# Performance work log

Measured on AMD Instinct MI355X. Metric: run time of the kernel, lower is better.

The kernel has to match this reference:

```python
import jax, jax.numpy as jnp
import numpy as np

N_NODES = 100000
N_EDGES = 1600000
IN_CH, HID_CH, LAT = 32, 32, 16


def _gcn_layer(h, W, b, src, dst, norm):
    # PyG GCNConv: h' = scatter_add(norm * (h W)[src] -> dst) + b
    h = h @ W                                   # [N, out]
    msg = h[src] * norm[:, None]                # [E+N, out] gather
    out = jax.ops.segment_sum(msg, dst, num_segments=N_NODES)
    return out + b


def setup_inputs() -> dict:
    key = jax.random.key(0)
    ks = jax.random.split(key, 8)
    x = jax.random.normal(ks[0], (N_NODES, IN_CH), dtype=jnp.float32)
    edge_index = jax.random.randint(ks[1], (2, N_EDGES), 0, N_NODES, dtype=jnp.int32)
    def glorot(k, fan_in, fan_out):
        lim = np.sqrt(6.0 / (fan_in + fan_out)).astype(np.float32)
        return jax.random.uniform(k, (fan_in, fan_out), jnp.float32, -lim, lim)
    return {
        "x": x,
        "edge_index": edge_index,
        "W1": glorot(ks[2], IN_CH, HID_CH),
        "b1": jnp.zeros((HID_CH,), jnp.float32),
        "Wmu": glorot(ks[3], HID_CH, LAT),
        "bmu": jnp.zeros((LAT,), jnp.float32),
        "Wlv": glorot(ks[4], HID_CH, LAT),
        "blv": jnp.zeros((LAT,), jnp.float32),
    }


def reference(x, edge_index, W1, b1, Wmu, bmu, Wlv, blv):
    # Add self-loops (GCNConv default add_self_loops=True)
    loops = jnp.arange(N_NODES, dtype=edge_index.dtype)
    src = jnp.concatenate([edge_index[0], loops])
    dst = jnp.concatenate([edge_index[1], loops])
    # Symmetric normalization: deg over destinations, norm = d^-1/2[src] * d^-1/2[dst]
    deg = jax.ops.segment_sum(jnp.ones_like(dst, dtype=x.dtype), dst,
                              num_segments=N_NODES)
    dinv = jnp.where(deg > 0, jax.lax.rsqrt(deg), 0.0)
    norm = dinv[src] * dinv[dst]                # [E+N]

    h = jax.nn.relu(_gcn_layer(x, W1, b1, src, dst, norm))
    mu = _gcn_layer(h, Wmu, bmu, src, dst, norm)
    logvar = _gcn_layer(h, Wlv, blv, src, dst, norm)
    return (mu, logvar)
```

## Files before the change

kernel.cpp:

```cpp
#include <hip/hip_runtime.h>
#include <hip/hip_fp16.h>

#define N_NODES 100000
#define N_EDGES 1600000
#define NCB 98
#define CAPC 17500
#define P1_CHUNK 2048
#define P1_BLOCKS 782
#define BK 64
#define NBF 1563
#define CAPF 1408
#define P2_SPLIT 16

__global__ __launch_bounds__(1024) void k_binit(int* __restrict__ cursor1,
                                                int* __restrict__ cursor2) {
    int i = blockIdx.x * 1024 + threadIdx.x;
    if (i < NCB) cursor1[i] = i * CAPC;
    if (i < NBF) cursor2[i] = i * CAPF;
}

__global__ __launch_bounds__(256) void k_part1(const int* __restrict__ src,
                                               const int* __restrict__ dst,
                                               int* __restrict__ cursor1,
                                               unsigned* __restrict__ packed1) {
    __shared__ int bh[NCB];
    __shared__ int base[NCB];
    int t = threadIdx.x;
    if (t < NCB) bh[t] = 0;
    __syncthreads();
    int e0 = blockIdx.x * P1_CHUNK;
    int e1 = e0 + P1_CHUNK; if (e1 > N_EDGES) e1 = N_EDGES;
    for (int e = e0 + t; e < e1; e += 256)
        atomicAdd(&bh[((unsigned)dst[e]) >> 10], 1);
    __syncthreads();
    if (t < NCB) {
        int c = bh[t];
        base[t] = (c > 0) ? atomicAdd(&cursor1[t], c) : 0;
        bh[t] = 0;
    }
    __syncthreads();
    for (int e = e0 + t; e < e1; e += 256) {
        unsigned d = (unsigned)dst[e];
        int b = d >> 10;
        int r = atomicAdd(&bh[b], 1);
        int pos = base[b] + r;
        if (pos < (b + 1) * CAPC)
            packed1[pos] = ((d & 1023u) << 17) | (unsigned)src[e];
    }
}

__global__ __launch_bounds__(256) void k_part2(const unsigned* __restrict__ packed1,
                                               const int* __restrict__ cursor1,
                                               int* __restrict__ cursor2,
                                               unsigned* __restrict__ packed2) {
    __shared__ int bh[16];
    __shared__ int base[16];
    int t = threadIdx.x;
    int c = blockIdx.x / P2_SPLIT;
    int k = blockIdx.x % P2_SPLIT;
    int cc = cursor1[c] - c * CAPC; if (cc > CAPC) cc = CAPC;
    int s0 = c * CAPC + (k * cc) / P2_SPLIT;
    int s1 = c * CAPC + ((k + 1) * cc) / P2_SPLIT;
    if (t < 16) bh[t] = 0;
    __syncthreads();
    for (int i = s0 + t; i < s1; i += 256)
        atomicAdd(&bh[(packed1[i] >> 17) >> 6], 1);
    __syncthreads();
    if (t < 16) {
        int cnt = bh[t];
        int fb = c * 16 + t;
        base[t] = (cnt > 0) ? atomicAdd(&cursor2[fb], cnt) : 0;
        bh[t] = 0;
    }
    __syncthreads();
    for (int i = s0 + t; i < s1; i += 256) {
        unsigned pk = packed1[i];
        unsigned dl = pk >> 17;
        int f = dl >> 6;
        int r = atomicAdd(&bh[f], 1);
        int pos = base[f] + r;
        int fb = c * 16 + f;
        if (pos < (fb + 1) * CAPF)
            packed2[pos] = ((dl & 63u) << 17) | (pk & 0x1FFFFu);
    }
}

__global__ __launch_bounds__(256) void k_csrx(const unsigned* __restrict__ packed2,
                                              const int* __restrict__ cursor2,
                                              const float* __restrict__ x,
                                              const float* __restrict__ W1,
                                              int* __restrict__ rowBeg,
                                              int* __restrict__ rowEnd,
                                              float* __restrict__ dinv,
                                              int* __restrict__ srcSorted,
                                              __half* __restrict__ p1) {
    __shared__ int cnt[BK];
    __shared__ int s[BK];
    __shared__ int cur[BK];
    __shared__ float sW[32 * 32];
    int t = threadIdx.x;
    int b = blockIdx.x;
    int seg0 = b * CAPF;
    int cc = cursor2[b] - seg0; if (cc > CAPF) cc = CAPF;
    int segEnd = seg0 + cc;
    if (t < BK) cnt[t] = 0;
    for (int i = t; i < 1024; i += 256) sW[i] = W1[i];
    __syncthreads();
    for (int i = seg0 + t; i < segEnd; i += 256)
        atomicAdd(&cnt[packed2[i] >> 17], 1);
    __syncthreads();
    int v = (t < BK) ? cnt[t] : 0;
    if (t < BK) s[t] = v;
    __syncthreads();
    for (int off = 1; off < BK; off <<= 1) {
        int u = (t < BK && t >= off) ? s[t - off] : 0;
        __syncthreads();
        if (t < BK) s[t] += u;
        __syncthreads();
    }
    int node = b * BK + t;
    if (t < BK) {
        int start = seg0 + s[t] - v;
        if (node < N_NODES) {
            rowBeg[node] = start;
            rowEnd[node] = start + v;
            dinv[node] = rsqrtf((float)(v + 1));
        }
        cur[t] = start;
    }
    __syncthreads();
    for (int i = seg0 + t; i < segEnd; i += 256) {
        unsigned pk = packed2[i];
        int pos = atomicAdd(&cur[pk >> 17], 1);
        srcSorted[pos] = (int)(pk & 0x1FFFFu);
    }
    int lane = t & 31;
    for (int r = (t >> 5); r < BK; r += 8) {
        int nd = b * BK + r;
        if (nd > N_NODES) break;
        if (nd == N_NODES) {
            p1[nd * 32 + lane] = __float2half(0.f);
            continue;
        }
        float xv = x[nd * 32 + lane];
        float a = 0.f;
#pragma unroll
        for (int k = 0; k < 32; ++k) {
            float xk = __shfl(xv, k, 32);
            a += xk * sW[k * 32 + lane];
        }
        float di = rsqrtf((float)(cnt[r] + 1));
        p1[nd * 32 + lane] = __float2half(di * a);
    }
}

__device__ __forceinline__ __half2 h2of(const float4& v, int c) {
    return reinterpret_cast<const __half2*>(&v)[c];
}

__device__ __forceinline__ void gatherRow4(const int* __restrict__ srcSorted,
                                           const float4* __restrict__ P,
                                           int beg, int end, int l,
                                           float* __restrict__ acc ) {
    for (int base = beg; base < end; base += 8) {
        int i0 = base + l, i1 = base + 4 + l;
        int sA = (i0 < end) ? srcSorted[i0] : N_NODES;
        int sB = (i1 < end) ? srcSorted[i1] : N_NODES;
        float4 v0 = P[__shfl(sA, 0, 4) * 4 + l];
        float4 v1 = P[__shfl(sA, 1, 4) * 4 + l];
        float4 v2 = P[__shfl(sA, 2, 4) * 4 + l];
        float4 v3 = P[__shfl(sA, 3, 4) * 4 + l];
        float4 v4 = P[__shfl(sB, 0, 4) * 4 + l];
        float4 v5 = P[__shfl(sB, 1, 4) * 4 + l];
        float4 v6 = P[__shfl(sB, 2, 4) * 4 + l];
        float4 v7 = P[__shfl(sB, 3, 4) * 4 + l];
#pragma unroll
        for (int c = 0; c < 4; ++c) {
            __half2 s01 = __hadd2(h2of(v0, c), h2of(v1, c));
            __half2 s23 = __hadd2(h2of(v2, c), h2of(v3, c));
            __half2 s45 = __hadd2(h2of(v4, c), h2of(v5, c));
            __half2 s67 = __hadd2(h2of(v6, c), h2of(v7, c));
            __half2 sum = __hadd2(__hadd2(s01, s23), __hadd2(s45, s67));
            float2 f = __half22float2(sum);
            acc[2 * c]     += f.x;
            acc[2 * c + 1] += f.y;
        }
    }
}

__global__ __launch_bounds__(256) void k_gx2(const int* __restrict__ rowBeg,
                                             const int* __restrict__ rowEnd,
                                             const int* __restrict__ srcSorted,
                                             const __half* __restrict__ p1,
                                             const float* __restrict__ dinv,
                                             const float* __restrict__ b1,
                                             const float* __restrict__ Wmu,
                                             const float* __restrict__ Wlv,
                                             __half* __restrict__ p2) {
    __shared__ float sW[32 * 32];
    __shared__ float sB[32];
    int t = threadIdx.x;
    for (int i = t; i < 1024; i += 256) {
        int k = i >> 5, oc = i & 31;
        sW[i] = (oc < 16) ? Wmu[k * 16 + oc] : Wlv[k * 16 + (oc - 16)];
    }
    if (t < 32) sB[t] = b1[t];
    __syncthreads();
    int l = t & 3;
    int node = blockIdx.x * 64 + (t >> 2);
    if (node > N_NODES) return;
    const float4* P = (const float4*)p1;
    if (node == N_NODES) {
        ((float4*)p2)[node * 4 + l] = make_float4(0.f, 0.f, 0.f, 0.f);
        return;
    }
    float acc[8] = {0.f, 0.f, 0.f, 0.f, 0.f, 0.f, 0.f, 0.f};
    gatherRow4(srcSorted, P, rowBeg[node], rowEnd[node], l, acc);
    float di = dinv[node];
    float4 ps = P[node * 4 + l];
    float h[8];
#pragma unroll
    for (int c = 0; c < 4; ++c) {
        float2 f = __half22float2(h2of(ps, c));
        h[2 * c]     = fmaxf(di * (acc[2 * c]     + f.x) + sB[8 * l + 2 * c],     0.f);
        h[2 * c + 1] = fmaxf(di * (acc[2 * c + 1] + f.y) + sB[8 * l + 2 * c + 1], 0.f);
    }
    float o[8] = {0.f, 0.f, 0.f, 0.f, 0.f, 0.f, 0.f, 0.f};
    const float4* W4 = (const float4*)sW;
#pragma unroll
    for (int m = 0; m < 4; ++m) {
#pragma unroll
        for (int j = 0; j < 8; ++j) {
            float hk = __shfl(h[j], m, 4);
            int k = 8 * m + j;
            float4 wa = W4[k * 8 + 2 * l];
            float4 wb = W4[k * 8 + 2 * l + 1];
            o[0] += hk * wa.x; o[1] += hk * wa.y; o[2] += hk * wa.z; o[3] += hk * wa.w;
            o[4] += hk * wb.x; o[5] += hk * wb.y; o[6] += hk * wb.z; o[7] += hk * wb.w;
        }
    }
    __half2 r0 = __floats2half2_rn(di * o[0], di * o[1]);
    __half2 r1 = __floats2half2_rn(di * o[2], di * o[3]);
    __half2 r2 = __floats2half2_rn(di * o[4], di * o[5]);
    __half2 r3 = __floats2half2_rn(di * o[6], di * o[7]);
    float4 st;
    st.x = *reinterpret_cast<float*>(&r0);
    st.y = *reinterpret_cast<float*>(&r1);
    st.z = *reinterpret_cast<float*>(&r2);
    st.w = *reinterpret_cast<float*>(&r3);
    ((float4*)p2)[node * 4 + l] = st;
}

__global__ __launch_bounds__(256) void k_gfin(const int* __restrict__ rowBeg,
                                              const int* __restrict__ rowEnd,
                                              const int* __restrict__ srcSorted,
                                              const __half* __restrict__ p2,
                                              const float* __restrict__ dinv,
                                              const float* __restrict__ bmu,
                                              const float* __restrict__ blv,
                                              float* __restrict__ out) {
    __shared__ float sB[32];
    int t = threadIdx.x;
    if (t < 32) sB[t] = (t < 16) ? bmu[t] : blv[t - 16];
    __syncthreads();
    int l = t & 3;
    int node = blockIdx.x * 64 + (t >> 2);
    if (node >= N_NODES) return;
    const float4* P = (const float4*)p2;
    float acc[8] = {0.f, 0.f, 0.f, 0.f, 0.f, 0.f, 0.f, 0.f};
    gatherRow4(srcSorted, P, rowBeg[node], rowEnd[node], l, acc);
    float di = dinv[node];
    float4 ps = P[node * 4 + l];
    float v[8];
#pragma unroll
    for (int c = 0; c < 4; ++c) {
        float2 f = __half22float2(h2of(ps, c));
        v[2 * c]     = di * (acc[2 * c]     + f.x) + sB[8 * l + 2 * c];
        v[2 * c + 1] = di * (acc[2 * c + 1] + f.y) + sB[8 * l + 2 * c + 1];
    }
    float4 o0 = make_float4(v[0], v[1], v[2], v[3]);
    float4 o1 = make_float4(v[4], v[5], v[6], v[7]);
    float4* dst = (l < 2) ? (float4*)out
                          : (float4*)(out + (size_t)N_NODES * 16);
    int base = node * 4 + (l & 1) * 2;
    dst[base]     = o0;
    dst[base + 1] = o1;
}

extern "C" void kernel_launch(void* const* d_in, const int* in_sizes, int n_in,
                              void* d_out, int out_size, void* d_ws, size_t ws_size,
                              hipStream_t stream) {
    const float* x   = (const float*)d_in[0];
    const int*   ei  = (const int*)d_in[1];
    const float* W1  = (const float*)d_in[2];
    const float* b1  = (const float*)d_in[3];
    const float* Wmu = (const float*)d_in[4];
    const float* bmu = (const float*)d_in[5];
    const float* Wlv = (const float*)d_in[6];
    const float* blv = (const float*)d_in[7];
    float* out = (float*)d_out;

    const int* src = ei;
    const int* dst = ei + N_EDGES;

    size_t off = 0;
    int* cursor1 = (int*)d_ws;                          off += NCB;
    int* cursor2 = (int*)d_ws + off;                    off += NBF;
    int* rowBeg  = (int*)d_ws + off;                    off += N_NODES;
    int* rowEnd  = (int*)d_ws + off;                    off += N_NODES;
    float* dinv  = (float*)((int*)d_ws + off);          off += N_NODES;
    off = (off + 63) & ~(size_t)63;
    unsigned* packed1 = (unsigned*)((int*)d_ws + off);  off += (size_t)NCB * CAPC;
    off = (off + 63) & ~(size_t)63;
    unsigned* packed2 = (unsigned*)((int*)d_ws + off);  off += (size_t)NBF * CAPF;
    off = (off + 63) & ~(size_t)63;
    int* srcSorted    = (int*)d_ws + off;
    __half* p1h       = (__half*)packed1;
    __half* p2h       = (__half*)packed2;

    const int gBlocks = 1563;

    k_binit<<<2, 1024, 0, stream>>>(cursor1, cursor2);
    k_part1<<<P1_BLOCKS, 256, 0, stream>>>(src, dst, cursor1, packed1);
    k_part2<<<NCB * P2_SPLIT, 256, 0, stream>>>(packed1, cursor1, cursor2, packed2);
    k_csrx <<<NBF, 256, 0, stream>>>(packed2, cursor2, x, W1,
                                     rowBeg, rowEnd, dinv, srcSorted, p1h);
    k_gx2  <<<gBlocks, 256, 0, stream>>>(rowBeg, rowEnd, srcSorted, p1h, dinv,
                                         b1, Wmu, Wlv, p2h);
    k_gfin <<<gBlocks, 256, 0, stream>>>(rowBeg, rowEnd, srcSorted, p2h, dinv,
                                         bmu, blv, out);
}
```

Baseline: 195.4 us.

## Fuse all stages into one cooperative persistent kernel with grid syncs

Combines cursor init, two partition passes, CSR build with the first linear transform, and both GCN gather layers into a single cooperatively launched kernel separated by grid-wide barriers. The grid is sized from the occupancy query and the CU count, and blocks loop over the former per-launch work items. This aims to remove inter-kernel launch gaps and tail effects. In exchange it adds grid.sync overhead, host-side occupancy queries each call, and possibly lower occupancy from the larger merged kernel. The old multi-kernel path is kept as a fallback if the cooperative launch fails.

After: 618.5 us. 3.16x slower.

```diff
diff --git a/kernel.cpp b/kernel.cpp
--- a/kernel.cpp
+++ b/kernel.cpp
@@ -1,158 +1,18 @@
 #include <hip/hip_runtime.h>
 #include <hip/hip_fp16.h>
+#include <hip/hip_cooperative_groups.h>
+
+namespace cg = cooperative_groups;
 
 #define N_NODES 100000
 #define N_EDGES 1600000
 #define NCB 98
 #define CAPC 17500
-#define P1_CHUNK 2048
-#define P1_BLOCKS 782
 #define BK 64
 #define NBF 1563
 #define CAPF 1408
-#define P2_SPLIT 16
-
-__global__ __launch_bounds__(1024) void k_binit(int* __restrict__ cursor1,
-                                                int* __restrict__ cursor2) {
-    int i = blockIdx.x * 1024 + threadIdx.x;
-    if (i < NCB) cursor1[i] = i * CAPC;
-    if (i < NBF) cursor2[i] = i * CAPF;
-}
-
-__global__ __launch_bounds__(256) void k_part1(const int* __restrict__ src,
-                                               const int* __restrict__ dst,
-                                               int* __restrict__ cursor1,
-                                               unsigned* __restrict__ packed1) {
-    __shared__ int bh[NCB];
-    __shared__ int base[NCB];
-    int t = threadIdx.x;
-    if (t < NCB) bh[t] = 0;
-    __syncthreads();
-    int e0 = blockIdx.x * P1_CHUNK;
-    int e1 = e0 + P1_CHUNK; if (e1 > N_EDGES) e1 = N_EDGES;
-    for (int e = e0 + t; e < e1; e += 256)
-        atomicAdd(&bh[((unsigned)dst[e]) >> 10], 1);
-    __syncthreads();
-    if (t < NCB) {
-        int c = bh[t];
-        base[t] = (c > 0) ? atomicAdd(&cursor1[t], c) : 0;
-        bh[t] = 0;
-    }
-    __syncthreads();
-    for (int e = e0 + t; e < e1; e += 256) {
-        unsigned d = (unsigned)dst[e];
-        int b = d >> 10;
-        int r = atomicAdd(&bh[b], 1);
-        int pos = base[b] + r;
-        if (pos < (b + 1) * CAPC)
-            packed1[pos] = ((d & 1023u) << 17) | (unsigned)src[e];
-    }
-}
-
-__global__ __launch_bounds__(256) void k_part2(const unsigned* __restrict__ packed1,
-                                               const int* __restrict__ cursor1,
-                                               int* __restrict__ cursor2,
-                                               unsigned* __restrict__ packed2) {
-    __shared__ int bh[16];
-    __shared__ int base[16];
-    int t = threadIdx.x;
-    int c = blockIdx.x / P2_SPLIT;
-    int k = blockIdx.x % P2_SPLIT;
-    int cc = cursor1[c] - c * CAPC; if (cc > CAPC) cc = CAPC;
-    int s0 = c * CAPC + (k * cc) / P2_SPLIT;
-    int s1 = c * CAPC + ((k + 1) * cc) / P2_SPLIT;
-    if (t < 16) bh[t] = 0;
-    __syncthreads();
-    for (int i = s0 + t; i < s1; i += 256)
-        atomicAdd(&bh[(packed1[i] >> 17) >> 6], 1);
-    __syncthreads();
-    if (t < 16) {
-        int cnt = bh[t];
-        int fb = c * 16 + t;
-        base[t] = (cnt > 0) ? atomicAdd(&cursor2[fb], cnt) : 0;
-        bh[t] = 0;
-    }
-    __syncthreads();
-    for (int i = s0 + t; i < s1; i += 256) {
-        unsigned pk = packed1[i];
-        unsigned dl = pk >> 17;
-        int f = dl >> 6;
-        int r = atomicAdd(&bh[f], 1);
-        int pos = base[f] + r;
-        int fb = c * 16 + f;
-        if (pos < (fb + 1) * CAPF)
-            packed2[pos] = ((dl & 63u) << 17) | (pk & 0x1FFFFu);
-    }
-}
-
-__global__ __launch_bounds__(256) void k_csrx(const unsigned* __restrict__ packed2,
-                                              const int* __restrict__ cursor2,
-                                              const float* __restrict__ x,
-                                              const float* __restrict__ W1,
-                                              int* __restrict__ rowBeg,
-                                              int* __restrict__ rowEnd,
-                                              float* __restrict__ dinv,
-                                              int* __restrict__ srcSorted,
-                                              __half* __restrict__ p1) {
-    __shared__ int cnt[BK];
-    __shared__ int s[BK];
-    __shared__ int cur[BK];
-    __shared__ float sW[32 * 32];
-    int t = threadIdx.x;
-    int b = blockIdx.x;
-    int seg0 = b * CAPF;
-    int cc = cursor2[b] - seg0; if (cc > CAPF) cc = CAPF;
-    int segEnd = seg0 + cc;
-    if (t < BK) cnt[t] = 0;
-    for (int i = t; i < 1024; i += 256) sW[i] = W1[i];
-    __syncthreads();
-    for (int i = seg0 + t; i < segEnd; i += 256)
-        atomicAdd(&cnt[packed2[i] >> 17], 1);
-    __syncthreads();
-    int v = (t < BK) ? cnt[t] : 0;
-    if (t < BK) s[t] = v;
-    __syncthreads();
-    for (int off = 1; off < BK; off <<= 1) {
-        int u = (t < BK && t >= off) ? s[t - off] : 0;
-        __syncthreads();
-        if (t < BK) s[t] += u;
-        __syncthreads();
-    }
-    int node = b * BK + t;
-    if (t < BK) {
-        int start = seg0 + s[t] - v;
-        if (node < N_NODES) {
-            rowBeg[node] = start;
-            rowEnd[node] = start + v;
-            dinv[node] = rsqrtf((float)(v + 1));
-        }
-        cur[t] = start;
-    }
-    __syncthreads();
-    for (int i = seg0 + t; i < segEnd; i += 256) {
-        unsigned pk = packed2[i];
-        int pos = atomicAdd(&cur[pk >> 17], 1);
-        srcSorted[pos] = (int)(pk & 0x1FFFFu);
-    }
-    int lane = t & 31;
-    for (int r = (t >> 5); r < BK; r += 8) {
-        int nd = b * BK + r;
-        if (nd > N_NODES) break;
-        if (nd == N_NODES) {
-            p1[nd * 32 + lane] = __float2half(0.f);
-            continue;
-        }
-        float xv = x[nd * 32 + lane];
-        float a = 0.f;
-#pragma unroll
-        for (int k = 0; k < 32; ++k) {
-            float xk = __shfl(xv, k, 32);
-            a += xk * sW[k * 32 + lane];
-        }
-        float di = rsqrtf((float)(cnt[r] + 1));
-        p1[nd * 32 + lane] = __float2half(di * a);
-    }
-}
+#define P1_CHUNK 2048
+#define NCH 782
 
 __device__ __forceinline__ __half2 h2of(const float4& v, int c) {
     return reinterpret_cast<const __half2*>(&v)[c];
@@ -188,6 +48,388 @@
     }
 }
 
+__global__ __launch_bounds__(256) void k_all(
+    const float* __restrict__ x,
+    const int* __restrict__ srcE,
+    const int* __restrict__ dstE,
+    const float* __restrict__ W1,
+    const float* __restrict__ b1,
+    const float* __restrict__ Wmu,
+    const float* __restrict__ bmu,
+    const float* __restrict__ Wlv,
+    const float* __restrict__ blv,
+    int* __restrict__ cursor1,
+    int* __restrict__ cursor2,
+    int* __restrict__ rowBeg,
+    int* __restrict__ rowEnd,
+    float* __restrict__ dinv,
+    unsigned* __restrict__ packed1,
+    unsigned* __restrict__ packed2,
+    int* __restrict__ srcSorted,
+    __half* __restrict__ p1,
+    __half* __restrict__ p2,
+    float* __restrict__ out)
+{
+    cg::grid_group grid = cg::this_grid();
+    __shared__ int bh[NCB];
+    __shared__ int base[NCB];
+    __shared__ int cnt[BK];
+    __shared__ int scn[BK];
+    __shared__ int cur[BK];
+    __shared__ float sW[1024];
+    __shared__ float sB[32];
+    int t = threadIdx.x;
+    int blk = blockIdx.x;
+    int G = gridDim.x;
+
+    for (int i = blk * 256 + t; i < NBF; i += G * 256) {
+        cursor2[i] = i * CAPF;
+        if (i < NCB) cursor1[i] = i * CAPC;
+    }
+    grid.sync();
+
+    for (int u = blk; u < NCH; u += G) {
+        __syncthreads();
+        if (t < NCB) bh[t] = 0;
+        __syncthreads();
+        int e0 = u * P1_CHUNK;
+        int e1 = e0 + P1_CHUNK; if (e1 > N_EDGES) e1 = N_EDGES;
+        for (int e = e0 + t; e < e1; e += 256)
+            atomicAdd(&bh[((unsigned)dstE[e]) >> 10], 1);
+        __syncthreads();
+        if (t < NCB) {
+            int c = bh[t];
+            base[t] = (c > 0) ? atomicAdd(&cursor1[t], c) : 0;
+            bh[t] = 0;
+        }
+        __syncthreads();
+        for (int e = e0 + t; e < e1; e += 256) {
+            unsigned d = (unsigned)dstE[e];
+            int b = d >> 10;
+            int r = atomicAdd(&bh[b], 1);
+            int pos = base[b] + r;
+            if (pos < (b + 1) * CAPC)
+                packed1[pos] = ((d & 1023u) << 17) | (unsigned)srcE[e];
+        }
+    }
+    grid.sync();
+
+    for (int u = blk; u < NCB * 16; u += G) {
+        __syncthreads();
+        int c = u >> 4;
+        int k = u & 15;
+        int cc = cursor1[c] - c * CAPC; if (cc > CAPC) cc = CAPC;
+        int s0 = c * CAPC + (k * cc) / 16;
+        int s1 = c * CAPC + ((k + 1) * cc) / 16;
+        if (t < 16) bh[t] = 0;
+        __syncthreads();
+        for (int i = s0 + t; i < s1; i += 256)
+            atomicAdd(&bh[(packed1[i] >> 17) >> 6], 1);
+        __syncthreads();
+        if (t < 16) {
+            int c2 = bh[t];
+            int fb = c * 16 + t;
+            base[t] = (c2 > 0) ? atomicAdd(&cursor2[fb], c2) : 0;
+            bh[t] = 0;
+        }
+        __syncthreads();
+        for (int i = s0 + t; i < s1; i += 256) {
+            unsigned pk = packed1[i];
+            unsigned dl = pk >> 17;
+            int f = dl >> 6;
+            int r = atomicAdd(&bh[f], 1);
+            int pos = base[f] + r;
+            int fb = c * 16 + f;
+            if (pos < (fb + 1) * CAPF)
+                packed2[pos] = ((dl & 63u) << 17) | (pk & 0x1FFFFu);
+        }
+    }
+    grid.sync();
+
+    for (int i = t; i < 1024; i += 256) sW[i] = W1[i];
+    for (int u = blk; u < NBF; u += G) {
+        __syncthreads();
+        if (t < BK) cnt[t] = 0;
+        __syncthreads();
+        int seg0 = u * CAPF;
+        int cc = cursor2[u] - seg0; if (cc > CAPF) cc = CAPF;
+        int segEnd = seg0 + cc;
+        for (int i = seg0 + t; i < segEnd; i += 256)
+            atomicAdd(&cnt[packed2[i] >> 17], 1);
+        __syncthreads();
+        int v = (t < BK) ? cnt[t] : 0;
+        if (t < BK) scn[t] = v;
+        __syncthreads();
+        for (int off = 1; off < BK; off <<= 1) {
+            int uu = (t < BK && t >= off) ? scn[t - off] : 0;
+            __syncthreads();
+            if (t < BK) scn[t] += uu;
+            __syncthreads();
+        }
+        int node = u * BK + t;
+        if (t < BK) {
+            int start = seg0 + scn[t] - v;
+            if (node < N_NODES) {
+                rowBeg[node] = start;
+                rowEnd[node] = start + v;
+                dinv[node] = rsqrtf((float)(v + 1));
+            }
+            cur[t] = start;
+        }
+        __syncthreads();
+        for (int i = seg0 + t; i < segEnd; i += 256) {
+            unsigned pk = packed2[i];
+            int pos = atomicAdd(&cur[pk >> 17], 1);
+            srcSorted[pos] = (int)(pk & 0x1FFFFu);
+        }
+        int lane = t & 31;
+        for (int r = (t >> 5); r < BK; r += 8) {
+            int nd = u * BK + r;
+            if (nd > N_NODES) break;
+            if (nd == N_NODES) {
+                p1[nd * 32 + lane] = __float2half(0.f);
+                continue;
+            }
+            float xv = x[nd * 32 + lane];
+            float a = 0.f;
+#pragma unroll
+            for (int k = 0; k < 32; ++k) {
+                float xk = __shfl(xv, k, 32);
+                a += xk * sW[k * 32 + lane];
+            }
+            float di = rsqrtf((float)(cnt[r] + 1));
+            p1[nd * 32 + lane] = __float2half(di * a);
+        }
+    }
+    grid.sync();
+
+    for (int i = t; i < 1024; i += 256) {
+        int k = i >> 5, oc = i & 31;
+        sW[i] = (oc < 16) ? Wmu[k * 16 + oc] : Wlv[k * 16 + (oc - 16)];
+    }
+    if (t < 32) sB[t] = b1[t];
+    __syncthreads();
+    {
+        int l = t & 3;
+        const float4* P = (const float4*)p1;
+        const float4* W4 = (const float4*)sW;
+        for (int u = blk; u < NBF; u += G) {
+            int node = u * 64 + (t >> 2);
+            if (node > N_NODES) continue;
+            if (node == N_NODES) {
+                ((float4*)p2)[node * 4 + l] = make_float4(0.f, 0.f, 0.f, 0.f);
+                continue;
+            }
+            float acc[8] = {0.f, 0.f, 0.f, 0.f, 0.f, 0.f, 0.f, 0.f};
+            gatherRow4(srcSorted, P, rowBeg[node], rowEnd[node], l, acc);
+            float di = dinv[node];
+            float4 ps = P[node * 4 + l];
+            float h[8];
+#pragma unroll
+            for (int c = 0; c < 4; ++c) {
+                float2 f = __half22float2(h2of(ps, c));
+                h[2 * c]     = fmaxf(di * (acc[2 * c]     + f.x) + sB[8 * l + 2 * c],     0.f);
+                h[2 * c + 1] = fmaxf(di * (acc[2 * c + 1] + f.y) + sB[8 * l + 2 * c + 1], 0.f);
+            }
+            float o[8] = {0.f, 0.f, 0.f, 0.f, 0.f, 0.f, 0.f, 0.f};
+#pragma unroll
+            for (int m = 0; m < 4; ++m) {
+#pragma unroll
+                for (int j = 0; j < 8; ++j) {
+                    float hk = __shfl(h[j], m, 4);
+                    int k = 8 * m + j;
+                    float4 wa = W4[k * 8 + 2 * l];
+                    float4 wb = W4[k * 8 + 2 * l + 1];
+                    o[0] += hk * wa.x; o[1] += hk * wa.y; o[2] += hk * wa.z; o[3] += hk * wa.w;
+                    o[4] += hk * wb.x; o[5] += hk * wb.y; o[6] += hk * wb.z; o[7] += hk * wb.w;
+                }
+            }
+            __half2 r0 = __floats2half2_rn(di * o[0], di * o[1]);
+            __half2 r1 = __floats2half2_rn(di * o[2], di * o[3]);
+            __half2 r2 = __floats2half2_rn(di * o[4], di * o[5]);
+            __half2 r3 = __floats2half2_rn(di * o[6], di * o[7]);
+            float4 st;
+            st.x = *reinterpret_cast<float*>(&r0);
+            st.y = *reinterpret_cast<float*>(&r1);
+            st.z = *reinterpret_cast<float*>(&r2);
+            st.w = *reinterpret_cast<float*>(&r3);
+            ((float4*)p2)[node * 4 + l] = st;
+        }
+    }
+    grid.sync();
+
+    if (t < 32) sB[t] = (t < 16) ? bmu[t] : blv[t - 16];
+    __syncthreads();
+    {
+        int l = t & 3;
+        const float4* P = (const float4*)p2;
+        for (int u = blk; u < NBF; u += G) {
+            int node = u * 64 + (t >> 2);
+            if (node >= N_NODES) continue;
+            float acc[8] = {0.f, 0.f, 0.f, 0.f, 0.f, 0.f, 0.f, 0.f};
+            gatherRow4(srcSorted, P, rowBeg[node], rowEnd[node], l, acc);
+            float di = dinv[node];
+            float4 ps = P[node * 4 + l];
+            float v[8];
+#pragma unroll
+            for (int c = 0; c < 4; ++c) {
+                float2 f = __half22float2(h2of(ps, c));
+                v[2 * c]     = di * (acc[2 * c]     + f.x) + sB[8 * l + 2 * c];
+                v[2 * c + 1] = di * (acc[2 * c + 1] + f.y) + sB[8 * l + 2 * c + 1];
+            }
+            float4 o0 = make_float4(v[0], v[1], v[2], v[3]);
+            float4 o1 = make_float4(v[4], v[5], v[6], v[7]);
+            float4* dst4 = (l < 2) ? (float4*)out
+                                   : (float4*)(out + (size_t)N_NODES * 16);
+            int b4 = node * 4 + (l & 1) * 2;
+            dst4[b4]     = o0;
+            dst4[b4 + 1] = o1;
+        }
+    }
+}
+
+__global__ __launch_bounds__(1024) void k_binit(int* __restrict__ cursor1,
+                                                int* __restrict__ cursor2) {
+    int i = blockIdx.x * 1024 + threadIdx.x;
+    if (i < NCB) cursor1[i] = i * CAPC;
+    if (i < NBF) cursor2[i] = i * CAPF;
+}
+
+__global__ __launch_bounds__(256) void k_part1(const int* __restrict__ src,
+                                               const int* __restrict__ dst,
+                                               int* __restrict__ cursor1,
+                                               unsigned* __restrict__ packed1) {
+    __shared__ int bh[NCB];
+    __shared__ int base[NCB];
+    int t = threadIdx.x;
+    if (t < NCB) bh[t] = 0;
+    __syncthreads();
+    int e0 = blockIdx.x * P1_CHUNK;
+    int e1 = e0 + P1_CHUNK; if (e1 > N_EDGES) e1 = N_EDGES;
+    for (int e = e0 + t; e < e1; e += 256)
+        atomicAdd(&bh[((unsigned)dst[e]) >> 10], 1);
+    __syncthreads();
+    if (t < NCB) {
+        int c = bh[t];
+        base[t] = (c > 0) ? atomicAdd(&cursor1[t], c) : 0;
+        bh[t] = 0;
+    }
+    __syncthreads();
+    for (int e = e0 + t; e < e1; e += 256) {
+        unsigned d = (unsigned)dst[e];
+        int b = d >> 10;
+        int r = atomicAdd(&bh[b], 1);
+        int pos = base[b] + r;
+        if (pos < (b + 1) * CAPC)
+            packed1[pos] = ((d & 1023u) << 17) | (unsigned)src[e];
+    }
+}
+
+__global__ __launch_bounds__(256) void k_part2(const unsigned* __restrict__ packed1,
+                                               const int* __restrict__ cursor1,
+                                               int* __restrict__ cursor2,
+                                               unsigned* __restrict__ packed2) {
+    __shared__ int bh[16];
+    __shared__ int base[16];
+    int t = threadIdx.x;
+    int c = blockIdx.x >> 4;
+    int k = blockIdx.x & 15;
+    int cc = cursor1[c] - c * CAPC; if (cc > CAPC) cc = CAPC;
+    int s0 = c * CAPC + (k * cc) / 16;
+    int s1 = c * CAPC + ((k + 1) * cc) / 16;
+    if (t < 16) bh[t] = 0;
+    __syncthreads();
+    for (int i = s0 + t; i < s1; i += 256)
+        atomicAdd(&bh[(packed1[i] >> 17) >> 6], 1);
+    __syncthreads();
+    if (t < 16) {
+        int cnt = bh[t];
+        int fb = c * 16 + t;
+        base[t] = (cnt > 0) ? atomicAdd(&cursor2[fb], cnt) : 0;
+        bh[t] = 0;
+    }
+    __syncthreads();
+    for (int i = s0 + t; i < s1; i += 256) {
+        unsigned pk = packed1[i];
+        unsigned dl = pk >> 17;
+        int f = dl >> 6;
+        int r = atomicAdd(&bh[f], 1);
+        int pos = base[f] + r;
+        int fb = c * 16 + f;
+        if (pos < (fb + 1) * CAPF)
+            packed2[pos] = ((dl & 63u) << 17) | (pk & 0x1FFFFu);
+    }
+}
+
+__global__ __launch_bounds__(256) void k_csrx(const unsigned* __restrict__ packed2,
+                                              const int* __restrict__ cursor2,
+                                              const float* __restrict__ x,
+                                              const float* __restrict__ W1,
+                                              int* __restrict__ rowBeg,
+                                              int* __restrict__ rowEnd,
+                                              float* __restrict__ dinv,
+                                              int* __restrict__ srcSorted,
+                                              __half* __restrict__ p1) {
+    __shared__ int cnt[BK];
+    __shared__ int scn[BK];
+    __shared__ int cur[BK];
+    __shared__ float sW[1024];
+    int t = threadIdx.x;
+    int b = blockIdx.x;
+    int seg0 = b * CAPF;
+    int cc = cursor2[b] - seg0; if (cc > CAPF) cc = CAPF;
+    int segEnd = seg0 + cc;
+    if (t < BK) cnt[t] = 0;
+    for (int i = t; i < 1024; i += 256) sW[i] = W1[i];
+    __syncthreads();
+    for (int i = seg0 + t; i < segEnd; i += 256)
+        atomicAdd(&cnt[packed2[i] >> 17], 1);
+    __syncthreads();
+    int v = (t < BK) ? cnt[t] : 0;
+    if (t < BK) scn[t] = v;
+    __syncthreads();
+    for (int off = 1; off < BK; off <<= 1) {
+        int u = (t < BK && t >= off) ? scn[t - off] : 0;
+        __syncthreads();
+        if (t < BK) scn[t] += u;
+        __syncthreads();
+    }
+    int node = b * BK + t;
+    if (t < BK) {
+        int start = seg0 + scn[t] - v;
+        if (node < N_NODES) {
+            rowBeg[node] = start;
+            rowEnd[node] = start + v;
+            dinv[node] = rsqrtf((float)(v + 1));
+        }
+        cur[t] = start;
+    }
+    __syncthreads();
+    for (int i = seg0 + t; i < segEnd; i += 256) {
+        unsigned pk = packed2[i];
+        int pos = atomicAdd(&cur[pk >> 17], 1);
+        srcSorted[pos] = (int)(pk & 0x1FFFFu);
+    }
+    int lane = t & 31;
+    for (int r = (t >> 5); r < BK; r += 8) {
+        int nd = b * BK + r;
+        if (nd > N_NODES) break;
+        if (nd == N_NODES) {
+            p1[nd * 32 + lane] = __float2half(0.f);
+            continue;
+        }
+        float xv = x[nd * 32 + lane];
+        float a = 0.f;
+#pragma unroll
+        for (int k = 0; k < 32; ++k) {
+            float xk = __shfl(xv, k, 32);
+            a += xk * sW[k * 32 + lane];
+        }
+        float di = rsqrtf((float)(cnt[r] + 1));
+        p1[nd * 32 + lane] = __float2half(di * a);
+    }
+}
+
 __global__ __launch_bounds__(256) void k_gx2(const int* __restrict__ rowBeg,
                                              const int* __restrict__ rowEnd,
                                              const int* __restrict__ srcSorted,
@@ -197,7 +439,7 @@
                                              const float* __restrict__ Wmu,
                                              const float* __restrict__ Wlv,
                                              __half* __restrict__ p2) {
-    __shared__ float sW[32 * 32];
+    __shared__ float sW[1024];
     __shared__ float sB[32];
     int t = threadIdx.x;
     for (int i = t; i < 1024; i += 256) {
@@ -280,11 +522,11 @@
     }
     float4 o0 = make_float4(v[0], v[1], v[2], v[3]);
     float4 o1 = make_float4(v[4], v[5], v[6], v[7]);
-    float4* dst = (l < 2) ? (float4*)out
-                          : (float4*)(out + (size_t)N_NODES * 16);
-    int base = node * 4 + (l & 1) * 2;
-    dst[base]     = o0;
-    dst[base + 1] = o1;
+    float4* dst4 = (l < 2) ? (float4*)out
+                           : (float4*)(out + (size_t)N_NODES * 16);
+    int b4 = node * 4 + (l & 1) * 2;
+    dst4[b4]     = o0;
+    dst4[b4 + 1] = o1;
 }
 
 extern "C" void kernel_launch(void* const* d_in, const int* in_sizes, int n_in,
@@ -318,15 +560,36 @@
     __half* p1h       = (__half*)packed1;
     __half* p2h       = (__half*)packed2;
 
-    const int gBlocks = 1563;
-
-    k_binit<<<2, 1024, 0, stream>>>(cursor1, cursor2);
-    k_part1<<<P1_BLOCKS, 256, 0, stream>>>(src, dst, cursor1, packed1);
-    k_part2<<<NCB * P2_SPLIT, 256, 0, stream>>>(packed1, cursor1, cursor2, packed2);
-    k_csrx <<<NBF, 256, 0, stream>>>(packed2, cursor2, x, W1,
-                                     rowBeg, rowEnd, dinv, srcSorted, p1h);
-    k_gx2  <<<gBlocks, 256, 0, stream>>>(rowBeg, rowEnd, srcSorted, p1h, dinv,
+    int dev = 0;
+    (void)hipGetDevice(&dev);
+    int numCU = 0;
+    (void)hipDeviceGetAttribute(&numCU, hipDeviceAttributeMultiprocessorCount, dev);
+    int occ = 0;
+    (void)hipOccupancyMaxActiveBlocksPerMultiprocessor(&occ, (const void*)k_all, 256, 0);
+    int grid = (numCU > 0 && occ > 0) ? numCU * occ : 0;
+    if (grid > 1568) grid = 1568;
+
+    hipError_t err = hipErrorUnknown;
+    if (grid > 0) {
+        void* kargs[] = {
+            (void*)&x, (void*)&src, (void*)&dst,
+            (void*)&W1, (void*)&b1, (void*)&Wmu, (void*)&bmu, (void*)&Wlv, (void*)&blv,
+            (void*)&cursor1, (void*)&cursor2, (void*)&rowBeg, (void*)&rowEnd, (void*)&dinv,
+            (void*)&packed1, (void*)&packed2, (void*)&srcSorted,
+            (void*)&p1h, (void*)&p2h, (void*)&out
+        };
+        err = hipLaunchCooperativeKernel((void*)k_all, dim3(grid), dim3(256),
+                                         kargs, 0, stream);
+    }
+    if (err != hipSuccess) {
+        k_binit<<<2, 1024, 0, stream>>>(cursor1, cursor2);
+        k_part1<<<NCH, 256, 0, stream>>>(src, dst, cursor1, packed1);
+        k_part2<<<NCB * 16, 256, 0, stream>>>(packed1, cursor1, cursor2, packed2);
+        k_csrx <<<NBF, 256, 0, stream>>>(packed2, cursor2, x, W1,
+                                         rowBeg, rowEnd, dinv, srcSorted, p1h);
+        k_gx2  <<<NBF, 256, 0, stream>>>(rowBeg, rowEnd, srcSorted, p1h, dinv,
                                          b1, Wmu, Wlv, p2h);
-    k_gfin <<<gBlocks, 256, 0, stream>>>(rowBeg, rowEnd, srcSorted, p2h, dinv,
+        k_gfin <<<NBF, 256, 0, stream>>>(rowBeg, rowEnd, srcSorted, p2h, dinv,
                                          bmu, blv, out);
-}
+    }
+}
```

## Drop second partition pass; CSR blocks filter their coarse bucket directly

Applied to the files above, without the earlier changes.

Removes the k_part2 kernel and the packed2 intermediate buffer. Each k_csrx block now scans the whole coarse bucket (about 16K entries) and keeps only the entries whose fine bucket matches its own, building the CSR directly from packed1. This saves one kernel launch plus a full write and read of the edge array. In exchange, each coarse bucket is read 16 times (twice per block), so global read traffic in the CSR kernel rises, though these reads likely hit L2.

Measured after the change: 226.6 us. +16.0%, slower.

```diff
diff --git a/kernel.cpp b/kernel.cpp
--- a/kernel.cpp
+++ b/kernel.cpp
@@ -6,153 +6,10 @@
 #define NCB 98
 #define CAPC 17500
 #define P1_CHUNK 2048
-#define P1_BLOCKS 782
+#define NCH 782
 #define BK 64
 #define NBF 1563
 #define CAPF 1408
-#define P2_SPLIT 16
-
-__global__ __launch_bounds__(1024) void k_binit(int* __restrict__ cursor1,
-                                                int* __restrict__ cursor2) {
-    int i = blockIdx.x * 1024 + threadIdx.x;
-    if (i < NCB) cursor1[i] = i * CAPC;
-    if (i < NBF) cursor2[i] = i * CAPF;
-}
-
-__global__ __launch_bounds__(256) void k_part1(const int* __restrict__ src,
-                                               const int* __restrict__ dst,
-                                               int* __restrict__ cursor1,
-                                               unsigned* __restrict__ packed1) {
-    __shared__ int bh[NCB];
-    __shared__ int base[NCB];
-    int t = threadIdx.x;
-    if (t < NCB) bh[t] = 0;
-    __syncthreads();
-    int e0 = blockIdx.x * P1_CHUNK;
-    int e1 = e0 + P1_CHUNK; if (e1 > N_EDGES) e1 = N_EDGES;
-    for (int e = e0 + t; e < e1; e += 256)
-        atomicAdd(&bh[((unsigned)dst[e]) >> 10], 1);
-    __syncthreads();
-    if (t < NCB) {
-        int c = bh[t];
-        base[t] = (c > 0) ? atomicAdd(&cursor1[t], c) : 0;
-        bh[t] = 0;
-    }
-    __syncthreads();
-    for (int e = e0 + t; e < e1; e += 256) {
-        unsigned d = (unsigned)dst[e];
-        int b = d >> 10;
-        int r = atomicAdd(&bh[b], 1);
-        int pos = base[b] + r;
-        if (pos < (b + 1) * CAPC)
-            packed1[pos] = ((d & 1023u) << 17) | (unsigned)src[e];
-    }
-}
-
-__global__ __launch_bounds__(256) void k_part2(const unsigned* __restrict__ packed1,
-                                               const int* __restrict__ cursor1,
-                                               int* __restrict__ cursor2,
-                                               unsigned* __restrict__ packed2) {
-    __shared__ int bh[16];
-    __shared__ int base[16];
-    int t = threadIdx.x;
-    int c = blockIdx.x / P2_SPLIT;
-    int k = blockIdx.x % P2_SPLIT;
-    int cc = cursor1[c] - c * CAPC; if (cc > CAPC) cc = CAPC;
-    int s0 = c * CAPC + (k * cc) / P2_SPLIT;
-    int s1 = c * CAPC + ((k + 1) * cc) / P2_SPLIT;
-    if (t < 16) bh[t] = 0;
-    __syncthreads();
-    for (int i = s0 + t; i < s1; i += 256)
-        atomicAdd(&bh[(packed1[i] >> 17) >> 6], 1);
-    __syncthreads();
-    if (t < 16) {
-        int cnt = bh[t];
-        int fb = c * 16 + t;
-        base[t] = (cnt > 0) ? atomicAdd(&cursor2[fb], cnt) : 0;
-        bh[t] = 0;
-    }
-    __syncthreads();
-    for (int i = s0 + t; i < s1; i += 256) {
-        unsigned pk = packed1[i];
-        unsigned dl = pk >> 17;
-        int f = dl >> 6;
-        int r = atomicAdd(&bh[f], 1);
-        int pos = base[f] + r;
-        int fb = c * 16 + f;
-        if (pos < (fb + 1) * CAPF)
-            packed2[pos] = ((dl & 63u) << 17) | (pk & 0x1FFFFu);
-    }
-}
-
-__global__ __launch_bounds__(256) void k_csrx(const unsigned* __restrict__ packed2,
-                                              const int* __restrict__ cursor2,
-                                              const float* __restrict__ x,
-                                              const float* __restrict__ W1,
-                                              int* __restrict__ rowBeg,
-                                              int* __restrict__ rowEnd,
-                                              float* __restrict__ dinv,
-                                              int* __restrict__ srcSorted,
-                                              __half* __restrict__ p1) {
-    __shared__ int cnt[BK];
-    __shared__ int s[BK];
-    __shared__ int cur[BK];
-    __shared__ float sW[32 * 32];
-    int t = threadIdx.x;
-    int b = blockIdx.x;
-    int seg0 = b * CAPF;
-    int cc = cursor2[b] - seg0; if (cc > CAPF) cc = CAPF;
-    int segEnd = seg0 + cc;
-    if (t < BK) cnt[t] = 0;
-    for (int i = t; i < 1024; i += 256) sW[i] = W1[i];
-    __syncthreads();
-    for (int i = seg0 + t; i < segEnd; i += 256)
-        atomicAdd(&cnt[packed2[i] >> 17], 1);
-    __syncthreads();
-    int v = (t < BK) ? cnt[t] : 0;
-    if (t < BK) s[t] = v;
-    __syncthreads();
-    for (int off = 1; off < BK; off <<= 1) {
-        int u = (t < BK && t >= off) ? s[t - off] : 0;
-        __syncthreads();
-        if (t < BK) s[t] += u;
-        __syncthreads();
-    }
-    int node = b * BK + t;
-    if (t < BK) {
-        int start = seg0 + s[t] - v;
-        if (node < N_NODES) {
-            rowBeg[node] = start;
-            rowEnd[node] = start + v;
-            dinv[node] = rsqrtf((float)(v + 1));
-        }
-        cur[t] = start;
-    }
-    __syncthreads();
-    for (int i = seg0 + t; i < segEnd; i += 256) {
-        unsigned pk = packed2[i];
-        int pos = atomicAdd(&cur[pk >> 17], 1);
-        srcSorted[pos] = (int)(pk & 0x1FFFFu);
-    }
-    int lane = t & 31;
-    for (int r = (t >> 5); r < BK; r += 8) {
-        int nd = b * BK + r;
-        if (nd > N_NODES) break;
-        if (nd == N_NODES) {
-            p1[nd * 32 + lane] = __float2half(0.f);
-            continue;
-        }
-        float xv = x[nd * 32 + lane];
-        float a = 0.f;
-#pragma unroll
-        for (int k = 0; k < 32; ++k) {
-            float xk = __shfl(xv, k, 32);
-            a += xk * sW[k * 32 + lane];
-        }
-        float di = rsqrtf((float)(cnt[r] + 1));
-        p1[nd * 32 + lane] = __float2half(di * a);
-    }
-}
 
 __device__ __forceinline__ __half2 h2of(const float4& v, int c) {
     return reinterpret_cast<const __half2*>(&v)[c];
@@ -188,6 +45,119 @@
     }
 }
 
+__global__ __launch_bounds__(128) void k_binit(int* __restrict__ cursor1) {
+    int t = threadIdx.x;
+    if (t < NCB) cursor1[t] = t * CAPC;
+}
+
+__global__ __launch_bounds__(256) void k_part1(const int* __restrict__ src,
+                                               const int* __restrict__ dst,
+                                               int* __restrict__ cursor1,
+                                               unsigned* __restrict__ packed1) {
+    __shared__ int bh[NCB];
+    __shared__ int base[NCB];
+    int t = threadIdx.x;
+    if (t < NCB) bh[t] = 0;
+    __syncthreads();
+    int e0 = blockIdx.x * P1_CHUNK;
+    int e1 = e0 + P1_CHUNK; if (e1 > N_EDGES) e1 = N_EDGES;
+    for (int e = e0 + t; e < e1; e += 256)
+        atomicAdd(&bh[((unsigned)dst[e]) >> 10], 1);
+    __syncthreads();
+    if (t < NCB) {
+        int c = bh[t];
+        base[t] = (c > 0) ? atomicAdd(&cursor1[t], c) : 0;
+        bh[t] = 0;
+    }
+    __syncthreads();
+    for (int e = e0 + t; e < e1; e += 256) {
+        unsigned d = (unsigned)dst[e];
+        int b = d >> 10;
+        int r = atomicAdd(&bh[b], 1);
+        int pos = base[b] + r;
+        if (pos < (b + 1) * CAPC)
+            packed1[pos] = ((d & 1023u) << 17) | (unsigned)src[e];
+    }
+}
+
+__global__ __launch_bounds__(256) void k_csrx(const unsigned* __restrict__ packed1,
+                                              const int* __restrict__ cursor1,
+                                              const float* __restrict__ x,
+                                              const float* __restrict__ W1,
+                                              int* __restrict__ rowBeg,
+                                              int* __restrict__ rowEnd,
+                                              float* __restrict__ dinv,
+                                              int* __restrict__ srcSorted,
+                                              __half* __restrict__ p1) {
+    __shared__ int cnt[BK];
+    __shared__ int scn[BK];
+    __shared__ int cur[BK];
+    __shared__ float sW[1024];
+    int t = threadIdx.x;
+    int b = blockIdx.x;
+    int c = b >> 4;
+    unsigned fl = (unsigned)(b & 15);
+    int seg0 = c * CAPC;
+    int cc = cursor1[c] - seg0; if (cc > CAPC) cc = CAPC;
+    int segEnd = seg0 + cc;
+    if (t < BK) cnt[t] = 0;
+    for (int i = t; i < 1024; i += 256) sW[i] = W1[i];
+    __syncthreads();
+    for (int i = seg0 + t; i < segEnd; i += 256) {
+        unsigned dl = packed1[i] >> 17;
+        if ((dl >> 6) == fl) atomicAdd(&cnt[dl & 63u], 1);
+    }
+    __syncthreads();
+    int v = (t < BK) ? cnt[t] : 0;
+    if (t < BK) scn[t] = v;
+    __syncthreads();
+    for (int off = 1; off < BK; off <<= 1) {
+        int u = (t < BK && t >= off) ? scn[t - off] : 0;
+        __syncthreads();
+        if (t < BK) scn[t] += u;
+        __syncthreads();
+    }
+    int fseg0 = b * CAPF;
+    int node = b * BK + t;
+    if (t < BK) {
+        int start = fseg0 + scn[t] - v;
+        if (node < N_NODES) {
+            rowBeg[node] = start;
+            rowEnd[node] = start + v;
+            dinv[node] = rsqrtf((float)(v + 1));
+        }
+        cur[t] = start;
+    }
+    __syncthreads();
+    for (int i = seg0 + t; i < segEnd; i += 256) {
+        unsigned pk = packed1[i];
+        unsigned dl = pk >> 17;
+        if ((dl >> 6) == fl) {
+            int pos = atomicAdd(&cur[dl & 63u], 1);
+            if (pos < (b + 1) * CAPF)
+                srcSorted[pos] = (int)(pk & 0x1FFFFu);
+        }
+    }
+    int lane = t & 31;
+    for (int r = (t >> 5); r < BK; r += 8) {
+        int nd = b * BK + r;
+        if (nd > N_NODES) break;
+        if (nd == N_NODES) {
+            p1[nd * 32 + lane] = __float2half(0.f);
+            continue;
+        }
+        float xv = x[nd * 32 + lane];
+        float a = 0.f;
+#pragma unroll
+        for (int k = 0; k < 32; ++k) {
+            float xk = __shfl(xv, k, 32);
+            a += xk * sW[k * 32 + lane];
+        }
+        float di = rsqrtf((float)(cnt[r] + 1));
+        p1[nd * 32 + lane] = __float2half(di * a);
+    }
+}
+
 __global__ __launch_bounds__(256) void k_gx2(const int* __restrict__ rowBeg,
                                              const int* __restrict__ rowEnd,
                                              const int* __restrict__ srcSorted,
@@ -197,7 +167,7 @@
                                              const float* __restrict__ Wmu,
                                              const float* __restrict__ Wlv,
                                              __half* __restrict__ p2) {
-    __shared__ float sW[32 * 32];
+    __shared__ float sW[1024];
     __shared__ float sB[32];
     int t = threadIdx.x;
     for (int i = t; i < 1024; i += 256) {
@@ -280,11 +250,11 @@
     }
     float4 o0 = make_float4(v[0], v[1], v[2], v[3]);
     float4 o1 = make_float4(v[4], v[5], v[6], v[7]);
-    float4* dst = (l < 2) ? (float4*)out
-                          : (float4*)(out + (size_t)N_NODES * 16);
-    int base = node * 4 + (l & 1) * 2;
-    dst[base]     = o0;
-    dst[base + 1] = o1;
+    float4* dst4 = (l < 2) ? (float4*)out
+                           : (float4*)(out + (size_t)N_NODES * 16);
+    int b4 = node * 4 + (l & 1) * 2;
+    dst4[b4]     = o0;
+    dst4[b4 + 1] = o1;
 }
 
 extern "C" void kernel_launch(void* const* d_in, const int* in_sizes, int n_in,
@@ -305,28 +275,23 @@
 
     size_t off = 0;
     int* cursor1 = (int*)d_ws;                          off += NCB;
-    int* cursor2 = (int*)d_ws + off;                    off += NBF;
     int* rowBeg  = (int*)d_ws + off;                    off += N_NODES;
     int* rowEnd  = (int*)d_ws + off;                    off += N_NODES;
     float* dinv  = (float*)((int*)d_ws + off);          off += N_NODES;
     off = (off + 63) & ~(size_t)63;
     unsigned* packed1 = (unsigned*)((int*)d_ws + off);  off += (size_t)NCB * CAPC;
     off = (off + 63) & ~(size_t)63;
-    unsigned* packed2 = (unsigned*)((int*)d_ws + off);  off += (size_t)NBF * CAPF;
+    int* srcSorted    = (int*)d_ws + off;               off += (size_t)NBF * CAPF;
     off = (off + 63) & ~(size_t)63;
-    int* srcSorted    = (int*)d_ws + off;
-    __half* p1h       = (__half*)packed1;
-    __half* p2h       = (__half*)packed2;
-
-    const int gBlocks = 1563;
-
-    k_binit<<<2, 1024, 0, stream>>>(cursor1, cursor2);
-    k_part1<<<P1_BLOCKS, 256, 0, stream>>>(src, dst, cursor1, packed1);
-    k_part2<<<NCB * P2_SPLIT, 256, 0, stream>>>(packed1, cursor1, cursor2, packed2);
-    k_csrx <<<NBF, 256, 0, stream>>>(packed2, cursor2, x, W1,
+    __half* p1h       = (__half*)((int*)d_ws + off);
+    __half* p2h       = (__half*)packed1;
+
+    k_binit<<<1, 128, 0, stream>>>(cursor1);
+    k_part1<<<NCH, 256, 0, stream>>>(src, dst, cursor1, packed1);
+    k_csrx <<<NBF, 256, 0, stream>>>(packed1, cursor1, x, W1,
                                      rowBeg, rowEnd, dinv, srcSorted, p1h);
-    k_gx2  <<<gBlocks, 256, 0, stream>>>(rowBeg, rowEnd, srcSorted, p1h, dinv,
-                                         b1, Wmu, Wlv, p2h);
-    k_gfin <<<gBlocks, 256, 0, stream>>>(rowBeg, rowEnd, srcSorted, p2h, dinv,
-                                         bmu, blv, out);
-}
+    k_gx2  <<<NBF, 256, 0, stream>>>(rowBeg, rowEnd, srcSorted, p1h, dinv,
+                                     b1, Wmu, Wlv, p2h);
+    k_gfin <<<NBF, 256, 0, stream>>>(rowBeg, rowEnd, srcSorted, p2h, dinv,
+                                     bmu, blv, out);
+}
```
